# Kernel tuning notes

Hardware: AMD Instinct MI355X
Metric: run time of the kernel (lower is better)

## Reference

```python
import jax, jax.numpy as jnp
import numpy as np
import math

B, N, P, S, C, NC = 8, 20000, 256, 32, 256, 18


def setup_inputs() -> dict:
    key = jax.random.key(0)
    ks = jax.random.split(key, 20)
    w = lambda k, shape: jax.random.normal(k, shape, jnp.float32) * 0.02
    return {
        "xyz": jax.random.normal(ks[0], (B, N, 3), jnp.float32),
        "features": jax.random.normal(ks[1], (B, C, N), jnp.float32),
        "boxes_size": jax.random.uniform(ks[2], (B, P, 3), jnp.float32, 0.2, 1.5),
        "boxes_label": jax.random.normal(ks[3], (B, P, NC), jnp.float32),
        "ts": jax.random.uniform(ks[4], (B,), jnp.float32) * 1000.0,
        "inds": jax.random.randint(ks[5], (B, P), 0, N, jnp.int32),
        # SharedMLP (259 -> 128 -> 128 -> 128), bn=False so conv1x1+bias+ReLU
        "mw0": w(ks[6], (128, C + 3)), "mb0": jnp.zeros((128,), jnp.float32),
        "mw1": w(ks[7], (128, 128)), "mb1": jnp.zeros((128,), jnp.float32),
        "mw2": w(ks[8], (128, 128)), "mb2": jnp.zeros((128,), jnp.float32),
        # label SharedMLP (18+128 -> 256 -> 256 -> 256)
        "lw0": w(ks[9], (256, NC + 128)), "lb0": jnp.zeros((256,), jnp.float32),
        "lw1": w(ks[10], (256, 256)), "lb1": jnp.zeros((256,), jnp.float32),
        "lw2": w(ks[11], (256, 256)), "lb2": jnp.zeros((256,), jnp.float32),
        # time_mlp: sinusoid(128) -> 512 -> GELU -> 512 ; block: SiLU -> 256
        "tw0": w(ks[12], (512, 128)), "tb0": jnp.zeros((512,), jnp.float32),
        "tw1": w(ks[13], (512, 512)), "tb1": jnp.zeros((512,), jnp.float32),
        "bw": w(ks[14], (256, 512)), "bb": jnp.zeros((256,), jnp.float32),
        # time_mlp_label: sinusoid(256) -> 1024 -> GELU -> 1024 ; block: SiLU -> 512
        "tlw0": w(ks[15], (1024, 256)), "tlb0": jnp.zeros((1024,), jnp.float32),
        "tlw1": w(ks[16], (1024, 1024)), "tlb1": jnp.zeros((1024,), jnp.float32),
        "blw": w(ks[17], (512, 1024)), "blb": jnp.zeros((512,), jnp.float32),
    }


def _sinusoid(t, dim):
    half = dim // 2
    freqs = jnp.exp(jnp.arange(half, dtype=jnp.float32) * (-(math.log(10000.0) / (half - 1))))
    e = t[:, None] * freqs[None, :]
    return jnp.concatenate([jnp.sin(e), jnp.cos(e)], axis=-1)


def _film(feat, ts, w0, b0, w1, b1, bw, bb, dim):
    # feat: [B, D, P]; replicates torch repeat_interleave/chunk/reshape exactly
    temb = jax.nn.gelu(_sinusoid(ts, dim) @ w0.T + b0, approximate=False) @ w1.T + b1
    ss = jax.nn.silu(temb) @ bw.T + bb          # [B, 2D]
    ss = jnp.repeat(ss, P, axis=0)              # [B*P, 2D]
    scale, shift = jnp.split(ss, 2, axis=1)
    scale = scale.reshape(-1, P)
    shift = shift.reshape(-1, P)
    f = feat.reshape(-1, P)
    return (f * (scale + 1.0) + shift).reshape(feat.shape[0], -1, P)


def reference(xyz, features, boxes_size, boxes_label, ts, inds,
              mw0, mb0, mw1, mb1, mw2, mb2,
              lw0, lb0, lw1, lb1, lw2, lb2,
              tw0, tb0, tw1, tb1, bw, bb,
              tlw0, tlb0, tlw1, tlb1, blw, blb):
    # gather proposal centers
    new_xyz = jnp.take_along_axis(xyz, inds[:, :, None], axis=1)        # [B,P,3]
    # axis-aligned box containment (the hull corners are an AABB: center +/- size/2)
    half = boxes_size * 0.5
    inside = jnp.all(jnp.abs(xyz[:, None, :, :] - new_xyz[:, :, None, :]) <= half[:, :, None, :], axis=-1)  # [B,P,N]
    # deterministic with-replacement sampling of in-box points: in-box indices first (stable sort), then cycle
    order = jnp.argsort(jnp.logical_not(inside), axis=-1)               # [B,P,N]
    count = jnp.maximum(inside.sum(axis=-1), 1)                          # [B,P]
    pos = jnp.arange(S, dtype=count.dtype)[None, None, :] % count[:, :, None]
    idx = jnp.take_along_axis(order, pos, axis=-1)                       # [B,P,S]
    b_idx = jnp.arange(B)[:, None, None]
    gxyz = xyz[b_idx, idx] - new_xyz[:, :, None, :]                      # [B,P,S,3]
    gfeat = jnp.transpose(features, (0, 2, 1))[b_idx, idx]               # [B,P,S,C]
    g = jnp.concatenate([gxyz, gfeat], axis=-1)                          # [B,P,S,3+C]
    act = lambda x, w, b: jax.nn.relu(jnp.einsum('bpsc,oc->bpso', x, w) + b)
    h = act(act(act(g, mw0, mb0), mw1, mb1), mw2, mb2)                   # [B,P,S,128]
    nf = h.max(axis=2)                                                   # [B,P,128] (max-pool over nsample)
    nf_t = jnp.transpose(nf, (0, 2, 1))                                  # [B,128,P]
    new_features = _film(nf_t, ts, tw0, tb0, tw1, tb1, bw, bb, 128)
    # label branch
    li = jnp.concatenate([boxes_label, nf], axis=-1)                     # [B,P,18+128]
    act2 = lambda x, w, b: jax.nn.relu(jnp.einsum('bpc,oc->bpo', x, w) + b)
    lf = act2(act2(act2(li, lw0, lb0), lw1, lb1), lw2, lb2)              # [B,P,256]
    lf_t = jnp.transpose(lf, (0, 2, 1))                                  # [B,256,P]
    label_feature = _film(lf_t, ts, tlw0, tlb0, tlw1, tlb1, blw, blb, 256)
    return (new_xyz, new_features, label_feature, inds)
```

## Files before the change

### kernel.cpp

```cpp
#include <hip/hip_runtime.h>
#include <math.h>

#define BB 8
#define NN 20000
#define PP 256
#define SSAMP 32
#define CC 256

typedef unsigned short u16;
typedef unsigned int u32;
typedef __attribute__((ext_vector_type(8))) short short8;
typedef __attribute__((ext_vector_type(4))) float f32x4;

struct __align__(4) f3v { float x, y, z; };

__device__ __forceinline__ float b2f(u16 u) {
    union { u32 i; float f; } x; x.i = ((u32)u) << 16; return x.f;
}
__device__ __forceinline__ u16 f2b(float f) {
    union { float f; u32 i; } x; x.f = f;
    u32 i = x.i;
    i += 0x7fffu + ((i >> 16) & 1u);
    return (u16)(i >> 16);
}
__device__ __forceinline__ float rnd_bf(float f) { return b2f(f2b(f)); }
__device__ __forceinline__ float geluf(float x) {
    return 0.5f * x * (1.0f + erff(x * 0.7071067811865476f));
}
__device__ __forceinline__ float siluf(float x) {
    return x / (1.0f + expf(-x));
}
__device__ __forceinline__ f32x4 fz4() { f32x4 z = {0.f,0.f,0.f,0.f}; return z; }

__device__ __forceinline__ float ldf(const void* p, size_t i, int f32f) {
    return f32f ? ((const float*)p)[i] : b2f(((const u16*)p)[i]);
}
__device__ __forceinline__ u16 ldw(const void* p, size_t i, int f32f) {
    return f32f ? f2b(((const float*)p)[i]) : ((const u16*)p)[i];
}

__device__ __forceinline__ int detect_f32d(const void* xyz) {
    int lane = threadIdx.x & 63;
    u16 u = ((const u16*)xyz)[(size_t)lane * 7496];
    int e = (u >> 7) & 0xFF;
    bool inR = (e >= 0x70) && (e <= 0x85);
    unsigned long long m = __ballot(inR);
    return (__popcll(m) < 48) ? 1 : 0;
}

__device__ __forceinline__ void repack_body(int f32f, int rb, int tid,
        const void* mw0, const void* mw1, const void* mw2,
        const void* lw0, const void* lw1, const void* lw2,
        const void* mb0, const void* mb1, const void* mb2,
        const void* lb0, const void* lb1, const void* lb2,
        u16* __restrict__ W0p, u16* __restrict__ W1p, u16* __restrict__ W2p,
        u16* __restrict__ L0p, u16* __restrict__ L1p, u16* __restrict__ L2p,
        float* __restrict__ biasF) {
    int i = rb * 256 + tid;
    if (i < 36864) {
        int o = i / 288, c = i % 288;
        u16 v = 0;
        if (c < 256) v = ldw(mw0, o * 259 + 3 + c, f32f);
        else if (c < 259) v = ldw(mw0, o * 259 + (c - 256), f32f);
        W0p[i] = v;
    } else if (i < 53248) {
        W1p[i - 36864] = ldw(mw1, i - 36864, f32f);
    } else if (i < 69632) {
        W2p[i - 53248] = ldw(mw2, i - 53248, f32f);
    } else if (i < 110592) {
        int j = i - 69632;
        int o = j / 160, c = j % 160;
        L0p[j] = (c < 146) ? ldw(lw0, o * 146 + c, f32f) : (u16)0;
    } else if (i < 176128) {
        L1p[i - 110592] = ldw(lw1, i - 110592, f32f);
    } else if (i < 241664) {
        L2p[i - 176128] = ldw(lw2, i - 176128, f32f);
    } else if (i < 242816) {
        int j = i - 241664;
        float v;
        if (j < 128) v = ldf(mb0, j, f32f);
        else if (j < 256) v = ldf(mb1, j - 128, f32f);
        else if (j < 384) v = ldf(mb2, j - 256, f32f);
        else if (j < 640) v = ldf(lb0, j - 384, f32f);
        else if (j < 896) v = ldf(lb1, j - 640, f32f);
        else v = ldf(lb2, j - 896, f32f);
        biasF[j] = v;
    }
}

__device__ __forceinline__ void transpose_body(int f32f, const void* __restrict__ feat,
        u16* __restrict__ featT, int n0i, int c0i, int bz, int b0, int tid,
        u16 (*tile)[66]) {
    int c0 = c0i * 64, n0 = n0i * 64;
    int b = b0 + bz;
    const size_t fb = (size_t)b * CC * NN;
    const size_t tb = (size_t)bz * NN * CC;
    if (n0 + 64 <= NN) {
        int n4 = tid & 15, ci = tid >> 4;
        if (f32f) {
            #pragma unroll
            for (int pass = 0; pass < 4; pass++) {
                int c = pass * 16 + ci;
                const float* src = (const float*)feat + fb + (size_t)(c0 + c) * NN + n0 + n4 * 4;
                float4 v = *(const float4*)src;
                tile[c][n4 * 4 + 0] = f2b(v.x);
                tile[c][n4 * 4 + 1] = f2b(v.y);
                tile[c][n4 * 4 + 2] = f2b(v.z);
                tile[c][n4 * 4 + 3] = f2b(v.w);
            }
        } else {
            #pragma unroll
            for (int pass = 0; pass < 4; pass++) {
                int c = pass * 16 + ci;
                const u16* src = (const u16*)feat + fb + (size_t)(c0 + c) * NN + n0 + n4 * 4;
                ushort4 v = *(const ushort4*)src;
                tile[c][n4 * 4 + 0] = v.x;
                tile[c][n4 * 4 + 1] = v.y;
                tile[c][n4 * 4 + 2] = v.z;
                tile[c][n4 * 4 + 3] = v.w;
            }
        }
        __syncthreads();
        int c4 = tid & 15, ni = tid >> 4;
        #pragma unroll
        for (int pass = 0; pass < 4; pass++) {
            int n = pass * 16 + ni;
            ushort4 o;
            o.x = tile[c4 * 4 + 0][n];
            o.y = tile[c4 * 4 + 1][n];
            o.z = tile[c4 * 4 + 2][n];
            o.w = tile[c4 * 4 + 3][n];
            *(ushort4*)(featT + tb + (size_t)(n0 + n) * CC + c0 + c4 * 4) = o;
        }
    } else {
        int tx = tid & 63, ty = tid >> 6;
        for (int i = 0; i < 16; i++) {
            int cl = ty * 16 + i;
            int n = n0 + tx;
            if (n < NN) tile[cl][tx] = ldw(feat, fb + (size_t)(c0 + cl) * NN + n, f32f);
        }
        __syncthreads();
        for (int i = 0; i < 16; i++) {
            int nl = ty * 16 + i;
            int n = n0 + nl;
            if (n < NN) featT[tb + (size_t)n * CC + c0 + tx] = tile[tx][nl];
        }
    }
}

template<int ACT, int SRC>
__device__ __forceinline__ void lin_body(int f32f, const void* __restrict__ xin,
        const void* __restrict__ W, const void* __restrict__ bias,
        float* __restrict__ out, int K, int O, int rb, int tid, float* xs) {
    if (SRC == 2) {
        const float* X = (const float*)xin;
        for (int i = tid; i < 8 * K; i += 256) xs[i] = X[i];
    } else {
        const int half = (SRC == 0) ? 64 : 128;
        const int dim = half * 2;
        const float cst = (SRC == 0) ? (logf(10000.f) / 63.f) : (logf(10000.f) / 127.f);
        for (int i = tid; i < 8 * dim; i += 256) {
            int b = i / dim, j = i % dim;
            float t = ldf(xin, b, f32f);
            int jj = (j < half) ? j : (j - half);
            float e = t * expf(-(float)jj * cst);
            xs[i] = (j < half) ? sinf(e) : cosf(e);
        }
    }
    __syncthreads();
    int lane = tid & 63, wv = tid >> 6;
    int r = rb * 4 + wv;
    if (r >= O) return;
    float acc[8] = {0.f, 0.f, 0.f, 0.f, 0.f, 0.f, 0.f, 0.f};
    for (int k = lane; k < K; k += 64) {
        float wval = ldf(W, (size_t)r * K + k, f32f);
        #pragma unroll
        for (int b = 0; b < 8; b++) acc[b] += wval * xs[b * K + k];
    }
    #pragma unroll
    for (int b = 0; b < 8; b++) {
        acc[b] += __shfl_xor(acc[b], 1);
        acc[b] += __shfl_xor(acc[b], 2);
        acc[b] += __shfl_xor(acc[b], 4);
        acc[b] += __shfl_xor(acc[b], 8);
        acc[b] += __shfl_xor(acc[b], 16);
        acc[b] += __shfl_xor(acc[b], 32);
    }
    if (lane == 0) {
        float bv = ldf(bias, r, f32f);
        #pragma unroll
        for (int b = 0; b < 8; b++) {
            float v = acc[b] + bv;
            if (ACT == 1) v = geluf(v);
            else if (ACT == 2) v = siluf(v);
            out[b * O + r] = v;
        }
    }
}

__device__ __forceinline__ void sample_body(int f32f, const void* __restrict__ xyz,
        const void* __restrict__ bsize, const int* __restrict__ inds,
        int* __restrict__ sidx, float* __restrict__ cenW,
        float* __restrict__ outXyz, float* __restrict__ outInds,
        int pg, int tid, int* sBuf, int* wcnt ) {
    int lane = tid & 63, w = tid >> 6;
    int b = pg >> 8;
    int ind = inds[pg];
    ind = ind < 0 ? 0 : (ind >= NN ? NN - 1 : ind);
    if (tid < SSAMP) sBuf[tid] = 0;
    size_t xb = (size_t)b * NN * 3;
    const f3v* Pts = (const f3v*)((const float*)xyz + xb);
    float cx, cy, cz;
    if (f32f) {
        f3v c = Pts[ind];
        cx = c.x; cy = c.y; cz = c.z;
    } else {
        cx = b2f(((const u16*)xyz)[xb + (size_t)ind * 3 + 0]);
        cy = b2f(((const u16*)xyz)[xb + (size_t)ind * 3 + 1]);
        cz = b2f(((const u16*)xyz)[xb + (size_t)ind * 3 + 2]);
    }
    float hx = 0.5f * ldf(bsize, pg * 3 + 0, f32f);
    float hy = 0.5f * ldf(bsize, pg * 3 + 1, f32f);
    float hz = 0.5f * ldf(bsize, pg * 3 + 2, f32f);
    int cnt = 0, par = 0;
    const unsigned long long lmask = (1ull << lane) - 1ull;
    for (int base = 0; base < NN; base += 4096, par ^= 64) {
        u32 inmask = 0;
        {
            float px[16], py[16], pz[16];
            #pragma unroll
            for (int u = 0; u < 16; u++) {
                int n = base + u * 256 + tid;
                int nc = n < NN ? n : NN - 1;
                if (f32f) {
                    f3v v = Pts[nc];
                    px[u] = v.x; py[u] = v.y; pz[u] = v.z;
                } else {
                    size_t a = xb + (size_t)nc * 3;
                    px[u] = b2f(((const u16*)xyz)[a]);
                    py[u] = b2f(((const u16*)xyz)[a + 1]);
                    pz[u] = b2f(((const u16*)xyz)[a + 2]);
                }
            }
            #pragma unroll
            for (int u = 0; u < 16; u++) {
                bool in_ = (base + u * 256 + tid < NN) &&
                           (fabsf(px[u] - cx) <= hx) &&
                           (fabsf(py[u] - cy) <= hy) &&
                           (fabsf(pz[u] - cz) <= hz);
                inmask |= ((u32)in_) << u;
            }
        }
        #pragma unroll
        for (int u = 0; u < 16; u++) {
            unsigned long long m = __ballot((inmask >> u) & 1u);
            if (lane == 0) wcnt[par + w * 16 + u] = (int)__popcll(m);
        }
        __syncthreads();
        int run = cnt;
        #pragma unroll
        for (int u = 0; u < 16; u++) {
            int c0 = wcnt[par + u];
            int c1 = wcnt[par + 16 + u];
            int c2 = wcnt[par + 32 + u];
            int c3 = wcnt[par + 48 + u];
            unsigned long long m = __ballot((inmask >> u) & 1u);
            if ((inmask >> u) & 1u) {
                int priorw = (w > 0 ? c0 : 0) + (w > 1 ? c1 : 0) + (w > 2 ? c2 : 0);
                int pos = run + priorw + (int)__popcll(m & lmask);
                if (pos < SSAMP) sBuf[pos] = base + u * 256 + tid;
            }
            run += c0 + c1 + c2 + c3;
        }
        cnt = run;
        if (cnt >= SSAMP) break;
    }
    __syncthreads();
    int ccap = cnt < SSAMP ? cnt : SSAMP;
    if (ccap < 1) ccap = 1;
    if (tid < SSAMP) sidx[pg * SSAMP + tid] = sBuf[tid % ccap];
    if (tid < 3) {
        float cv = tid == 0 ? cx : (tid == 1 ? cy : cz);
        outXyz[pg * 3 + tid] = cv;
        cenW[pg * 3 + tid] = cv;
    }
    if (tid == 0) outInds[pg] = rnd_bf((float)ind);
}

__device__ __forceinline__ void mlp1_body(int f32f,
        const u16* __restrict__ featT, const void* __restrict__ feat,
        int pbase, int tier,
        const void* __restrict__ xyz, const int* __restrict__ sidx,
        const float* __restrict__ cenW,
        const u16* __restrict__ W0p, const u16* __restrict__ W1p,
        const u16* __restrict__ W2p, const float* __restrict__ biasF,
        u16* __restrict__ nfB, float* __restrict__ nfF,
        int tid, u16* gA, int* nrowS, float* centS) {
    int b = pbase >> 8;
    if (tid < 64) {
        int n = sidx[pbase * SSAMP + tid];
        nrowS[tid] = n < 0 ? 0 : (n >= NN ? NN - 1 : n);
    }
    if (tid < 6) centS[tid] = cenW[pbase * 3 + tid];
    for (int e = tid; e < 64 * 32; e += 256) {
        int row = e >> 5, c2 = e & 31;
        if (c2 >= 8 && c2 < 28)
            *(u32*)&gA[row * 296 + 256 + (c2 - 8) * 2] = 0u;
    }
    __syncthreads();
    if (tier >= 1) {
        size_t rowBase = (tier == 2) ? ((size_t)b * NN) : 0;
        for (int e = tid; e < 64 * 32; e += 256) {
            int row = e >> 5, seg = e & 31;
            int n = nrowS[row];
            uint4 v = *(const uint4*)(featT + (rowBase + n) * CC + seg * 8);
            *(uint4*)&gA[row * 296 + seg * 8] = v;
        }
    } else {
        int row = tid & 63;
        int n = nrowS[row];
        const size_t fb = (size_t)b * CC * NN;
        int cbase = tid >> 6;
        for (int it = 0; it < 64; it++) {
            int cch = it * 4 + cbase;
            gA[row * 296 + cch] = ldw(feat, fb + (size_t)cch * NN + n, f32f);
        }
    }
    if (tid < 64) {
        int row = tid, q = row >> 5;
        int n = nrowS[row];
        size_t a = ((size_t)b * NN + n) * 3;
        for (int d = 0; d < 3; d++) {
            float gv = ldf(xyz, a + d, f32f) - centS[q * 3 + d];
            gA[row * 296 + 256 + d] = f2b(gv);
        }
    }
    __syncthreads();

    int lane = tid & 63, w = tid >> 6;
    int c15 = lane & 15, kq = lane >> 4;
    f32x4 acc[4][2];

    for (int mt = 0; mt < 4; mt++) for (int j = 0; j < 2; j++) acc[mt][j] = fz4();
    for (int ks = 0; ks < 9; ks++) {
        int k0 = ks * 32 + kq * 8;
        short8 af[4];
        for (int mt = 0; mt < 4; mt++)
            af[mt] = *(const short8*)&gA[(mt * 16 + c15) * 296 + k0];
        for (int j = 0; j < 2; j++) {
            int col = w * 32 + j * 16 + c15;
            short8 bf = *(const short8*)(W0p + col * 288 + k0);
            for (int mt = 0; mt < 4; mt++)
                acc[mt][j] = __builtin_amdgcn_mfma_f32_16x16x32_bf16(af[mt], bf, acc[mt][j], 0, 0, 0);
        }
    }
    __syncthreads();
    u16* h1s = gA;
    u16* h2s = gA + 8704;
    for (int j = 0; j < 2; j++) {
        int col = w * 32 + j * 16 + c15;
        float bias = biasF[col];
        for (int mt = 0; mt < 4; mt++)
            for (int r = 0; r < 4; r++) {
                float v = acc[mt][j][r] + bias;
                v = v > 0.f ? v : 0.f;
                h1s[(mt * 16 + kq * 4 + r) * 136 + col] = f2b(v);
            }
    }
    __syncthreads();

    for (int mt = 0; mt < 4; mt++) for (int j = 0; j < 2; j++) acc[mt][j] = fz4();
    for (int ks = 0; ks < 4; ks++) {
        int k0 = ks * 32 + kq * 8;
        short8 af[4];
        for (int mt = 0; mt < 4; mt++)
            af[mt] = *(const short8*)&h1s[(mt * 16 + c15) * 136 + k0];
        for (int j = 0; j < 2; j++) {
            int col = w * 32 + j * 16 + c15;
            short8 bf = *(const short8*)(W1p + col * 128 + k0);
            for (int mt = 0; mt < 4; mt++)
                acc[mt][j] = __builtin_amdgcn_mfma_f32_16x16x32_bf16(af[mt], bf, acc[mt][j], 0, 0, 0);
        }
    }
    __syncthreads();
    for (int j = 0; j < 2; j++) {
        int col = w * 32 + j * 16 + c15;
        float bias = biasF[128 + col];
        for (int mt = 0; mt < 4; mt++)
            for (int r = 0; r < 4; r++) {
                float v = acc[mt][j][r] + bias;
                v = v > 0.f ? v : 0.f;
                h2s[(mt * 16 + kq * 4 + r) * 136 + col] = f2b(v);
            }
    }
    __syncthreads();

    for (int mt = 0; mt < 4; mt++) for (int j = 0; j < 2; j++) acc[mt][j] = fz4();
    for (int ks = 0; ks < 4; ks++) {
        int k0 = ks * 32 + kq * 8;
        short8 af[4];
        for (int mt = 0; mt < 4; mt++)
            af[mt] = *(const short8*)&h2s[(mt * 16 + c15) * 136 + k0];
        for (int j = 0; j < 2; j++) {
            int col = w * 32 + j * 16 + c15;
            short8 bf = *(const short8*)(W2p + col * 128 + k0);
            for (int mt = 0; mt < 4; mt++)
                acc[mt][j] = __builtin_amdgcn_mfma_f32_16x16x32_bf16(af[mt], bf, acc[mt][j], 0, 0, 0);
        }
    }
    int pA = pbase & 255, pB = (pbase + 1) & 255;
    for (int j = 0; j < 2; j++) {
        int col = w * 32 + j * 16 + c15;
        float bias = biasF[256 + col];
        float mA = 0.f, mB = 0.f;
        for (int mt = 0; mt < 2; mt++)
            for (int r = 0; r < 4; r++) {
                float v = acc[mt][j][r] + bias; v = v > 0.f ? v : 0.f;
                mA = fmaxf(mA, v);
            }
        for (int mt = 2; mt < 4; mt++)
            for (int r = 0; r < 4; r++) {
                float v = acc[mt][j][r] + bias; v = v > 0.f ? v : 0.f;
                mB = fmaxf(mB, v);
            }
        mA = fmaxf(mA, __shfl_xor(mA, 16)); mA = fmaxf(mA, __shfl_xor(mA, 32));
        mB = fmaxf(mB, __shfl_xor(mB, 16)); mB = fmaxf(mB, __shfl_xor(mB, 32));
        if (lane < 16) {
            nfB[(size_t)(pbase + 0) * 128 + col] = f2b(mA);
            nfB[(size_t)(pbase + 1) * 128 + col] = f2b(mB);
            nfF[((size_t)b * 128 + col) * 256 + pA] = mA;
            nfF[((size_t)b * 128 + col) * 256 + pB] = mB;
        }
    }
}

__global__ __launch_bounds__(256) void k_front(
        const void* __restrict__ xyz, const void* __restrict__ feat,
        const void* __restrict__ bsize, const int* __restrict__ inds,
        const void* __restrict__ ts,
        const void* mw0, const void* mw1, const void* mw2,
        const void* lw0, const void* lw1, const void* lw2,
        const void* mb0, const void* mb1, const void* mb2,
        const void* lb0, const void* lb1, const void* lb2,
        const void* tw0, const void* tb0,
        const void* tlw0, const void* tlb0,
        u16* __restrict__ featT, int nTrans,
        int* __restrict__ sidx, float* __restrict__ cenW,
        float* __restrict__ outXyz, float* __restrict__ outInds,
        u16* __restrict__ W0p, u16* __restrict__ W1p, u16* __restrict__ W2p,
        u16* __restrict__ L0p, u16* __restrict__ L1p, u16* __restrict__ L2p,
        float* __restrict__ biasF, float* __restrict__ h0W, float* __restrict__ g0W) {
    __shared__ __align__(16) char smem[8448];
    int tid = threadIdx.x;
    int f32f = detect_f32d(xyz);
    unsigned bx = blockIdx.x;
    if (nTrans > 0) {
        const unsigned NI = 7u * 2048u;
        if (bx < NI) {
            if (bx % 7u == 0u) {
                sample_body(f32f, xyz, bsize, inds, sidx, cenW, outXyz, outInds,
                            (int)(bx / 7u), tid, (int*)smem, (int*)(smem + 128));
            } else {
                int t = (int)(bx - bx / 7u - 1u);
                if (t < nTrans)
                    transpose_body(f32f, feat, featT, t % 313, (t / 313) & 3, t / 1252,
                                   0, tid, (u16(*)[66])smem);
            }
        } else if (bx < NI + 949u) {
            repack_body(f32f, (int)(bx - NI), tid, mw0, mw1, mw2, lw0, lw1, lw2,
                        mb0, mb1, mb2, lb0, lb1, lb2, W0p, W1p, W2p, L0p, L1p, L2p, biasF);
        } else if (bx < NI + 1077u) {
            lin_body<1, 0>(f32f, ts, tw0, tb0, h0W, 128, 512, (int)(bx - NI - 949u), tid, (float*)smem);
        } else {
            lin_body<1, 1>(f32f, ts, tlw0, tlb0, g0W, 256, 1024, (int)(bx - NI - 1077u), tid, (float*)smem);
        }
    } else {
        if (bx < 2048u) {
            sample_body(f32f, xyz, bsize, inds, sidx, cenW, outXyz, outInds,
                        (int)bx, tid, (int*)smem, (int*)(smem + 128));
        } else if (bx < 2997u) {
            repack_body(f32f, (int)(bx - 2048u), tid, mw0, mw1, mw2, lw0, lw1, lw2,
                        mb0, mb1, mb2, lb0, lb1, lb2, W0p, W1p, W2p, L0p, L1p, L2p, biasF);
        } else if (bx < 3125u) {
            lin_body<1, 0>(f32f, ts, tw0, tb0, h0W, 128, 512, (int)(bx - 2997u), tid, (float*)smem);
        } else {
            lin_body<1, 1>(f32f, ts, tlw0, tlb0, g0W, 256, 1024, (int)(bx - 3125u), tid, (float*)smem);
        }
    }
}

__global__ __launch_bounds__(256) void k_mid(int nMlp, int blockOff, int tier,
        const u16* __restrict__ featT, const void* __restrict__ feat,
        const void* __restrict__ xyz, const int* __restrict__ sidx,
        const float* __restrict__ cenW,
        const u16* __restrict__ W0p, const u16* __restrict__ W1p,
        const u16* __restrict__ W2p, const float* __restrict__ biasF,
        u16* __restrict__ nfB, float* __restrict__ nfF,
        const void* tw1, const void* tb1, const void* tlw1, const void* tlb1,
        const float* __restrict__ h0W, const float* __restrict__ g0W,
        float* __restrict__ tembW, float* __restrict__ temblW) {
    __shared__ __align__(16) char smem[38176];
    int tid = threadIdx.x;
    int f32f = detect_f32d(xyz);
    int bx = (int)blockIdx.x;
    if (bx < nMlp) {
        mlp1_body(f32f, featT, feat, (bx + blockOff) * 2, tier, xyz, sidx, cenW,
                  W0p, W1p, W2p, biasF, nfB, nfF, tid,
                  (u16*)smem, (int*)(smem + 37888), (float*)(smem + 38144));
    } else {
        int lb = bx - nMlp;
        float* xs = (float*)smem;
        if (lb < 128) lin_body<2, 2>(f32f, h0W, tw1, tb1, tembW, 512, 512, lb, tid, xs);
        else lin_body<2, 2>(f32f, g0W, tlw1, tlb1, temblW, 1024, 1024, lb - 128, tid, xs);
    }
}

__global__ __launch_bounds__(256) void k_lin3(const void* __restrict__ xyz,
        const void* bw, const void* bb, const void* blw, const void* blb,
        const float* __restrict__ tembW, const float* __restrict__ temblW,
        float* __restrict__ ssW, float* __restrict__ sslW) {
    __shared__ float xs[8 * 1024];
    int tid = threadIdx.x;
    int f32f = detect_f32d(xyz);
    unsigned bx = blockIdx.x;
    if (bx < 64u) lin_body<0, 2>(f32f, tembW, bw, bb, ssW, 512, 256, (int)bx, tid, xs);
    else lin_body<0, 2>(f32f, temblW, blw, blb, sslW, 1024, 512, (int)(bx - 64u), tid, xs);
}

__global__ __launch_bounds__(256) void k_transpose(const void* __restrict__ xyz,
                                                   const void* __restrict__ feat,
                                                   u16* __restrict__ featT, int b0) {
    __shared__ u16 tile[64][66];
    int f32f = detect_f32d(xyz);
    transpose_body(f32f, feat, featT, blockIdx.x, blockIdx.y, blockIdx.z, b0,
                   threadIdx.x, tile);
}

__global__ __launch_bounds__(256) void k_tail(const void* __restrict__ xyz,
        const void* __restrict__ blabel,
        const u16* __restrict__ nfB, const u16* __restrict__ L0p,
        const u16* __restrict__ L1p, const u16* __restrict__ L2p,
        const float* __restrict__ biasF, const float* __restrict__ sslW,
        const float* __restrict__ ssW, const float* __restrict__ nfF,
        float* __restrict__ outLF, float* __restrict__ outNF) {
    __shared__ u16 liS[16 * 168];
    __shared__ u16 h1L[16 * 264];
    __shared__ u16 h2L[16 * 264];
    int f32f = detect_f32d(xyz);
    int tid = threadIdx.x;
    unsigned bxu = blockIdx.x;
    if (bxu >= 128u) {
        int base = (int)(bxu - 128u) * 4096;
        #pragma unroll
        for (int i = 0; i < 16; i++) {
            int idx = base + i * 256 + tid;
            int p = idx & 255;
            int cb = idx >> 8;
            int b = cb >> 7;
            float sc = ssW[b * 256 + (p & 127)] + 1.f;
            float sh = ssW[b * 256 + 128 + (p & 127)];
            outNF[idx] = nfF[idx] * sc + sh;
        }
        return;
    }
    int pbase = (int)bxu * 16;
    for (int e = tid; e < 16 * 160; e += 256) {
        int row = e / 160, c = e % 160;
        int pg = pbase + row;
        u16 v = 0;
        if (c < 18) v = ldw(blabel, pg * 18 + c, f32f);
        else if (c < 146) v = nfB[(size_t)pg * 128 + (c - 18)];
        liS[row * 168 + c] = v;
    }
    __syncthreads();
    int lane = tid & 63, w = tid >> 6;
    int c15 = lane & 15, kq = lane >> 4;
    f32x4 acc[4];

    for (int j = 0; j < 4; j++) acc[j] = fz4();
    for (int ks = 0; ks < 5; ks++) {
        int k0 = ks * 32 + kq * 8;
        short8 af = *(const short8*)&liS[c15 * 168 + k0];
        for (int j = 0; j < 4; j++) {
            int col = w * 64 + j * 16 + c15;
            short8 bf = *(const short8*)(L0p + col * 160 + k0);
            acc[j] = __builtin_amdgcn_mfma_f32_16x16x32_bf16(af, bf, acc[j], 0, 0, 0);
        }
    }
    for (int j = 0; j < 4; j++) {
        int col = w * 64 + j * 16 + c15;
        float bias = biasF[384 + col];
        for (int r = 0; r < 4; r++) {
            float v = acc[j][r] + bias; v = v > 0.f ? v : 0.f;
            h1L[(kq * 4 + r) * 264 + col] = f2b(v);
        }
    }
    __syncthreads();

    for (int j = 0; j < 4; j++) acc[j] = fz4();
    for (int ks = 0; ks < 8; ks++) {
        int k0 = ks * 32 + kq * 8;
        short8 af = *(const short8*)&h1L[c15 * 264 + k0];
        for (int j = 0; j < 4; j++) {
            int col = w * 64 + j * 16 + c15;
            short8 bf = *(const short8*)(L1p + col * 256 + k0);
            acc[j] = __builtin_amdgcn_mfma_f32_16x16x32_bf16(af, bf, acc[j], 0, 0, 0);
        }
    }
    for (int j = 0; j < 4; j++) {
        int col = w * 64 + j * 16 + c15;
        float bias = biasF[640 + col];
        for (int r = 0; r < 4; r++) {
            float v = acc[j][r] + bias; v = v > 0.f ? v : 0.f;
            h2L[(kq * 4 + r) * 264 + col] = f2b(v);
        }
    }
    __syncthreads();

    for (int j = 0; j < 4; j++) acc[j] = fz4();
    for (int ks = 0; ks < 8; ks++) {
        int k0 = ks * 32 + kq * 8;
        short8 af = *(const short8*)&h2L[c15 * 264 + k0];
        for (int j = 0; j < 4; j++) {
            int col = w * 64 + j * 16 + c15;
            short8 bf = *(const short8*)(L2p + col * 256 + k0);
            acc[j] = __builtin_amdgcn_mfma_f32_16x16x32_bf16(af, bf, acc[j], 0, 0, 0);
        }
    }
    for (int j = 0; j < 4; j++) {
        int col = w * 64 + j * 16 + c15;
        float bias = biasF[896 + col];
        for (int r = 0; r < 4; r++) {
            int pr = pbase + kq * 4 + r;
            int bb2 = pr >> 8, p = pr & 255;
            float v = acc[j][r] + bias; v = v > 0.f ? v : 0.f;
            float sc = sslW[bb2 * 512 + p] + 1.f;
            float sh = sslW[bb2 * 512 + 256 + p];
            outLF[((size_t)bb2 * 256 + col) * 256 + p] = v * sc + sh;
        }
    }
}

extern "C" void kernel_launch(void* const* d_in, const int* in_sizes, int n_in,
                              void* d_out, int out_size, void* d_ws, size_t ws_size,
                              hipStream_t stream) {
    const void* xyz    = d_in[0];
    const void* feat   = d_in[1];
    const void* bsize  = d_in[2];
    const void* blabel = d_in[3];
    const void* ts     = d_in[4];
    const int* inds    = (const int*)d_in[5];
    const void* mw0 = d_in[6];  const void* mb0 = d_in[7];
    const void* mw1 = d_in[8];  const void* mb1 = d_in[9];
    const void* mw2 = d_in[10]; const void* mb2 = d_in[11];
    const void* lw0 = d_in[12]; const void* lb0 = d_in[13];
    const void* lw1 = d_in[14]; const void* lb1 = d_in[15];
    const void* lw2 = d_in[16]; const void* lb2 = d_in[17];
    const void* tw0 = d_in[18]; const void* tb0 = d_in[19];
    const void* tw1 = d_in[20]; const void* tb1 = d_in[21];
    const void* bw  = d_in[22]; const void* bb  = d_in[23];
    const void* tlw0 = d_in[24]; const void* tlb0 = d_in[25];
    const void* tlw1 = d_in[26]; const void* tlb1 = d_in[27];
    const void* blw  = d_in[28]; const void* blb  = d_in[29];

    float* out = (float*)d_out;
    float* outXyz  = out;
    float* outNF   = out + 6144;
    float* outLF   = out + 268288;
    float* outInds = out + 792576;

    char* ws = (char*)d_ws;
    u16*   W0p   = (u16*)(ws + 64);
    u16*   W1p   = (u16*)(ws + 73792);
    u16*   W2p   = (u16*)(ws + 106560);
    u16*   L0p   = (u16*)(ws + 139328);
    u16*   L1p   = (u16*)(ws + 221248);
    u16*   L2p   = (u16*)(ws + 352320);
    float* biasF = (float*)(ws + 483392);
    float* ssW   = (float*)(ws + 488000);
    float* sslW  = (float*)(ws + 496192);
    float* cenW  = (float*)(ws + 512576);
    int*   sidx  = (int*)(ws + 537152);
    u16*   nfB   = (u16*)(ws + 799296);
    float* h0W   = (float*)(ws + 1323584);
    float* tembW = (float*)(ws + 1339968);
    float* g0W   = (float*)(ws + 1356352);
    float* temblW= (float*)(ws + 1389120);
    float* nfF   = (float*)(ws + 1421888);
    u16*   featT = (u16*)(ws + 2470464);
    const size_t NEED_A = 2470464ull + 81920000ull;
    const size_t NEED_B = 2470464ull + 10240000ull;
    int tier = (ws_size >= NEED_A) ? 2 : ((ws_size >= NEED_B) ? 1 : 0);

    int nTrans = (tier == 2) ? 10016 : 0;
    unsigned gFront = (nTrans > 0) ? (7u * 2048u + 949u + 384u)
                                   : (2048u + 949u + 384u);
    k_front<<<dim3(gFront), dim3(256), 0, stream>>>(
        xyz, feat, bsize, inds, ts,
        mw0, mw1, mw2, lw0, lw1, lw2,
        mb0, mb1, mb2, lb0, lb1, lb2,
        tw0, tb0, tlw0, tlb0,
        featT, nTrans, sidx, cenW, outXyz, outInds,
        W0p, W1p, W2p, L0p, L1p, L2p, biasF, h0W, g0W);

    if (tier == 2) {
        k_mid<<<dim3(1024 + 384), dim3(256), 0, stream>>>(1024, 0, 2,
            featT, feat, xyz, sidx, cenW, W0p, W1p, W2p, biasF, nfB, nfF,
            tw1, tb1, tlw1, tlb1, h0W, g0W, tembW, temblW);
    } else if (tier == 1) {
        for (int b = 0; b < BB; b++) {
            k_transpose<<<dim3(313, 4, 1), dim3(256), 0, stream>>>(xyz, feat, featT, b);
            k_mid<<<dim3(128), dim3(256), 0, stream>>>(128, b * 128, 1,
                featT, feat, xyz, sidx, cenW, W0p, W1p, W2p, biasF, nfB, nfF,
                tw1, tb1, tlw1, tlb1, h0W, g0W, tembW, temblW);
        }
        k_mid<<<dim3(384), dim3(256), 0, stream>>>(0, 0, 1,
            featT, feat, xyz, sidx, cenW, W0p, W1p, W2p, biasF, nfB, nfF,
            tw1, tb1, tlw1, tlb1, h0W, g0W, tembW, temblW);
    } else {
        k_mid<<<dim3(1024 + 384), dim3(256), 0, stream>>>(1024, 0, 0,
            featT, feat, xyz, sidx, cenW, W0p, W1p, W2p, biasF, nfB, nfF,
            tw1, tb1, tlw1, tlb1, h0W, g0W, tembW, temblW);
    }

    k_lin3<<<dim3(192), dim3(256), 0, stream>>>(xyz, bw, bb, blw, blb,
                                                tembW, temblW, ssW, sslW);

    k_tail<<<dim3(128 + 64), dim3(256), 0, stream>>>(xyz, blabel, nfB,
        L0p, L1p, L2p, biasF, sslW, ssW, nfF, outLF, outNF);
}
```

Measured before the change: 430.6 us.

## Split point sampling out of the fused front kernel into its own launch

```diff
diff --git a/kernel.cpp b/kernel.cpp
--- a/kernel.cpp
+++ b/kernel.cpp
@@ -198,12 +198,17 @@
     }
 }
 
-__device__ __forceinline__ void sample_body(int f32f, const void* __restrict__ xyz,
-        const void* __restrict__ bsize, const int* __restrict__ inds,
+__global__ __launch_bounds__(256) void k_sample(
+        const void* __restrict__ xyz, const void* __restrict__ bsize,
+        const int* __restrict__ inds,
         int* __restrict__ sidx, float* __restrict__ cenW,
-        float* __restrict__ outXyz, float* __restrict__ outInds,
-        int pg, int tid, int* sBuf, int* wcnt ) {
+        float* __restrict__ outXyz, float* __restrict__ outInds) {
+    __shared__ int sBuf[SSAMP];
+    __shared__ int wcnt[128];
+    int f32f = detect_f32d(xyz);
+    int tid = threadIdx.x;
     int lane = tid & 63, w = tid >> 6;
+    int pg = (int)blockIdx.x;
     int b = pg >> 8;
     int ind = inds[pg];
     ind = ind < 0 ? 0 : (ind >= NN ? NN - 1 : ind);
@@ -434,9 +439,8 @@
     }
 }
 
-__global__ __launch_bounds__(256) void k_front(
+__global__ __launch_bounds__(256) void k_trans(
         const void* __restrict__ xyz, const void* __restrict__ feat,
-        const void* __restrict__ bsize, const int* __restrict__ inds,
         const void* __restrict__ ts,
         const void* mw0, const void* mw1, const void* mw2,
         const void* lw0, const void* lw1, const void* lw2,
@@ -445,47 +449,27 @@
         const void* tw0, const void* tb0,
         const void* tlw0, const void* tlb0,
         u16* __restrict__ featT, int nTrans,
-        int* __restrict__ sidx, float* __restrict__ cenW,
-        float* __restrict__ outXyz, float* __restrict__ outInds,
         u16* __restrict__ W0p, u16* __restrict__ W1p, u16* __restrict__ W2p,
         u16* __restrict__ L0p, u16* __restrict__ L1p, u16* __restrict__ L2p,
         float* __restrict__ biasF, float* __restrict__ h0W, float* __restrict__ g0W) {
-    __shared__ __align__(16) char smem[8448];
+    __shared__ __align__(16) char smem[32768];
     int tid = threadIdx.x;
     int f32f = detect_f32d(xyz);
     unsigned bx = blockIdx.x;
-    if (nTrans > 0) {
-        const unsigned NI = 7u * 2048u;
-        if (bx < NI) {
-            if (bx % 7u == 0u) {
-                sample_body(f32f, xyz, bsize, inds, sidx, cenW, outXyz, outInds,
-                            (int)(bx / 7u), tid, (int*)smem, (int*)(smem + 128));
-            } else {
-                int t = (int)(bx - bx / 7u - 1u);
-                if (t < nTrans)
-                    transpose_body(f32f, feat, featT, t % 313, (t / 313) & 3, t / 1252,
-                                   0, tid, (u16(*)[66])smem);
-            }
-        } else if (bx < NI + 949u) {
-            repack_body(f32f, (int)(bx - NI), tid, mw0, mw1, mw2, lw0, lw1, lw2,
-                        mb0, mb1, mb2, lb0, lb1, lb2, W0p, W1p, W2p, L0p, L1p, L2p, biasF);
-        } else if (bx < NI + 1077u) {
-            lin_body<1, 0>(f32f, ts, tw0, tb0, h0W, 128, 512, (int)(bx - NI - 949u), tid, (float*)smem);
-        } else {
-            lin_body<1, 1>(f32f, ts, tlw0, tlb0, g0W, 256, 1024, (int)(bx - NI - 1077u), tid, (float*)smem);
-        }
+    unsigned s1 = (unsigned)nTrans;
+    unsigned s2 = s1 + 949u;
+    unsigned s3 = s2 + 128u;
+    if (bx < s1) {
+        int t = (int)bx;
+        transpose_body(f32f, feat, featT, t % 313, (t / 313) & 3, t / 1252, 0, tid,
+                       (u16(*)[66])smem);
+    } else if (bx < s2) {
+        repack_body(f32f, (int)(bx - s1), tid, mw0, mw1, mw2, lw0, lw1, lw2,
+                    mb0, mb1, mb2, lb0, lb1, lb2, W0p, W1p, W2p, L0p, L1p, L2p, biasF);
+    } else if (bx < s3) {
+        lin_body<1, 0>(f32f, ts, tw0, tb0, h0W, 128, 512, (int)(bx - s2), tid, (float*)smem);
     } else {
-        if (bx < 2048u) {
-            sample_body(f32f, xyz, bsize, inds, sidx, cenW, outXyz, outInds,
-                        (int)bx, tid, (int*)smem, (int*)(smem + 128));
-        } else if (bx < 2997u) {
-            repack_body(f32f, (int)(bx - 2048u), tid, mw0, mw1, mw2, lw0, lw1, lw2,
-                        mb0, mb1, mb2, lb0, lb1, lb2, W0p, W1p, W2p, L0p, L1p, L2p, biasF);
-        } else if (bx < 3125u) {
-            lin_body<1, 0>(f32f, ts, tw0, tb0, h0W, 128, 512, (int)(bx - 2997u), tid, (float*)smem);
-        } else {
-            lin_body<1, 1>(f32f, ts, tlw0, tlb0, g0W, 256, 1024, (int)(bx - 3125u), tid, (float*)smem);
-        }
+        lin_body<1, 1>(f32f, ts, tlw0, tlb0, g0W, 256, 1024, (int)(bx - s3), tid, (float*)smem);
     }
 }
 
@@ -692,15 +676,16 @@
     const size_t NEED_B = 2470464ull + 10240000ull;
     int tier = (ws_size >= NEED_A) ? 2 : ((ws_size >= NEED_B) ? 1 : 0);
 
+    k_sample<<<dim3(2048), dim3(256), 0, stream>>>(xyz, bsize, inds,
+                                                   sidx, cenW, outXyz, outInds);
+
     int nTrans = (tier == 2) ? 10016 : 0;
-    unsigned gFront = (nTrans > 0) ? (7u * 2048u + 949u + 384u)
-                                   : (2048u + 949u + 384u);
-    k_front<<<dim3(gFront), dim3(256), 0, stream>>>(
-        xyz, feat, bsize, inds, ts,
+    k_trans<<<dim3((unsigned)nTrans + 949u + 384u), dim3(256), 0, stream>>>(
+        xyz, feat, ts,
         mw0, mw1, mw2, lw0, lw1, lw2,
         mb0, mb1, mb2, lb0, lb1, lb2,
         tw0, tb0, tlw0, tlb0,
-        featT, nTrans, sidx, cenW, outXyz, outInds,
+        featT, nTrans,
         W0p, W1p, W2p, L0p, L1p, L2p, biasF, h0W, g0W);
 
     if (tier == 2) {
```

New measurement: 448.3 us. 1.04x slower.
